# Kernel tuning notes

Measured on AMD Instinct MI355X. Metric: run time of the kernel, lower is better.

## Reference

```python
import jax, jax.numpy as jnp
import numpy as np

N_ATOMS = 1_000_000
N_PAIRS = 32_000_000
N_MOL = 10_000

def setup_inputs() -> dict:
    key = jax.random.key(0)
    k1, k2, k3, k4, k5 = jax.random.split(key, 5)
    charges = jax.random.normal(k1, (N_ATOMS, 1), dtype=jnp.float32)
    # distances in [0.5, 2.5) to avoid divide-by-zero
    pair_dist = jax.random.uniform(k2, (N_PAIRS,), dtype=jnp.float32, minval=0.5, maxval=2.5)
    pair_first = jax.random.randint(k3, (N_PAIRS,), 0, N_ATOMS)
    pair_second = jax.random.randint(k4, (N_PAIRS,), 0, N_ATOMS)
    mol_index = jax.random.randint(k5, (N_ATOMS,), 0, N_MOL)
    return {
        "charges": charges,
        "pair_dist": pair_dist,
        "pair_first": pair_first,
        "pair_second": pair_second,
        "mol_index": mol_index,
        "n_molecules": N_MOL,
        "energy_conversion_factor": jnp.float32(14.399645),
    }

def reference(charges, pair_dist, pair_first, pair_second, mol_index, n_molecules, energy_conversion_factor):
    n_atoms = charges.shape[0]
    # gather charge of second atom in each pair, scale by 1/r  -> [n_pairs, 1]
    voltage_pairs = energy_conversion_factor * (charges[pair_second] / pair_dist[:, None])
    # scatter-add pair voltages onto first atom -> [n_atoms, 1]
    voltage_atom = jax.ops.segment_sum(voltage_pairs, pair_first, num_segments=n_atoms)
    # per-atom coulomb energy, then segment-sum over molecules
    coulomb_atom = voltage_atom * charges
    coulomb_molecules = 0.5 * jax.ops.segment_sum(coulomb_atom, mol_index, num_segments=n_molecules)
    return coulomb_molecules, voltage_atom
```

## Files before the change

### kernel.cpp

```cpp
#include <hip/hip_runtime.h>
#include <hip/hip_fp16.h>

#define BUCKET_BITS 12
#define BUCKET_SIZE 4096
#define NB 256
#define PPB 8192
#define BLK_A 256
#define MOL_BLOCKS 64


__global__ void init_cursors(int* __restrict__ cur, int nbuckets, int cap) {
    int b = blockIdx.x * blockDim.x + threadIdx.x;
    if (b < nbuckets) cur[b] = b * cap;
}

__global__ __launch_bounds__(BLK_A) void pair_scatter(
    const int4*   __restrict__ first4,
    const int4*   __restrict__ second4,
    const float4* __restrict__ dist4,
    const float*  __restrict__ charges,
    const float*  __restrict__ ecf_p,
    int* __restrict__ cur,
    unsigned* __restrict__ entries,
    int n_pairs4) {
    __shared__ unsigned stag[PPB];
    __shared__ int hist[NB];
    __shared__ int scanA[NB];
    __shared__ int lofs[NB + 1];
    __shared__ int gadj[NB];

    const int tid = threadIdx.x;
    hist[tid] = 0;
    __syncthreads();

    const int groups = PPB / 4;
    const int base4 = blockIdx.x * groups;

    #pragma unroll
    for (int it = 0; it < groups / BLK_A; ++it) {
        int g = base4 + it * BLK_A + tid;
        if (g < n_pairs4) {
            int4 f = first4[g];
            atomicAdd(&hist[f.x >> BUCKET_BITS], 1);
            atomicAdd(&hist[f.y >> BUCKET_BITS], 1);
            atomicAdd(&hist[f.z >> BUCKET_BITS], 1);
            atomicAdd(&hist[f.w >> BUCKET_BITS], 1);
        }
    }
    __syncthreads();

    scanA[tid] = hist[tid];
    __syncthreads();
    for (int off = 1; off < NB; off <<= 1) {
        int v = scanA[tid];
        if (tid >= off) v += scanA[tid - off];
        __syncthreads();
        scanA[tid] = v;
        __syncthreads();
    }
    if (tid == 0) lofs[0] = 0;
    lofs[tid + 1] = scanA[tid];
    __syncthreads();

    int cnt = hist[tid];
    if (cnt > 0) gadj[tid] = atomicAdd(&cur[tid], cnt) - lofs[tid];
    hist[tid] = lofs[tid];
    __syncthreads();

    const float ecf = *ecf_p;

    #pragma unroll
    for (int it = 0; it < groups / BLK_A; ++it) {
        int g = base4 + it * BLK_A + tid;
        if (g < n_pairs4) {
            int4   f = first4[g];
            int4   s = second4[g];
            float4 d = dist4[g];
            float v0 = ecf * charges[s.x] / d.x;
            float v1 = ecf * charges[s.y] / d.y;
            float v2 = ecf * charges[s.z] / d.z;
            float v3 = ecf * charges[s.w] / d.w;
            int p0 = atomicAdd(&hist[f.x >> BUCKET_BITS], 1);
            stag[p0] = ((unsigned)(f.x & (BUCKET_SIZE - 1)) << 16) |
                       (unsigned)__half_as_ushort(__float2half(v0));
            int p1 = atomicAdd(&hist[f.y >> BUCKET_BITS], 1);
            stag[p1] = ((unsigned)(f.y & (BUCKET_SIZE - 1)) << 16) |
                       (unsigned)__half_as_ushort(__float2half(v1));
            int p2 = atomicAdd(&hist[f.z >> BUCKET_BITS], 1);
            stag[p2] = ((unsigned)(f.z & (BUCKET_SIZE - 1)) << 16) |
                       (unsigned)__half_as_ushort(__float2half(v2));
            int p3 = atomicAdd(&hist[f.w >> BUCKET_BITS], 1);
            stag[p3] = ((unsigned)(f.w & (BUCKET_SIZE - 1)) << 16) |
                       (unsigned)__half_as_ushort(__float2half(v3));
        }
    }
    __syncthreads();

    const int tot = lofs[NB];
    for (int i = tid; i < tot; i += BLK_A) {
        unsigned e = stag[i];
        int lo = 0, hi = NB - 1;
        #pragma unroll
        for (int s = 0; s < 8; ++s) {
            int mid = (lo + hi + 1) >> 1;
            if (lofs[mid] <= i) lo = mid; else hi = mid - 1;
        }
        entries[gadj[lo] + i] = e;
    }
}

__global__ __launch_bounds__(1024) void bucket_reduce(
    const unsigned* __restrict__ entries,
    const int* __restrict__ cur,
    float* __restrict__ voltage,
    int cap, int n_atoms) {
    __shared__ float volt[BUCKET_SIZE];
    const int b = blockIdx.x;
    for (int i = threadIdx.x; i < BUCKET_SIZE; i += blockDim.x) volt[i] = 0.f;
    __syncthreads();
    const int start = b * cap;
    const int end = cur[b];
    const int cnt = end - start;
    const int cnt4 = cnt >> 2;
    const uint4* e4p = (const uint4*)(entries + start);
    for (int i = threadIdx.x; i < cnt4; i += blockDim.x) {
        uint4 e = e4p[i];
        atomicAdd(&volt[e.x >> 16], __half2float(__ushort_as_half((unsigned short)(e.x & 0xFFFFu))));
        atomicAdd(&volt[e.y >> 16], __half2float(__ushort_as_half((unsigned short)(e.y & 0xFFFFu))));
        atomicAdd(&volt[e.z >> 16], __half2float(__ushort_as_half((unsigned short)(e.z & 0xFFFFu))));
        atomicAdd(&volt[e.w >> 16], __half2float(__ushort_as_half((unsigned short)(e.w & 0xFFFFu))));
    }
    for (int i = (cnt4 << 2) + threadIdx.x; i < cnt; i += blockDim.x) {
        unsigned e = entries[start + i];
        atomicAdd(&volt[e >> 16], __half2float(__ushort_as_half((unsigned short)(e & 0xFFFFu))));
    }
    __syncthreads();
    const int abase = b << BUCKET_BITS;
    const int nat = min(BUCKET_SIZE, n_atoms - abase);
    for (int i = threadIdx.x; i < nat; i += blockDim.x)
        voltage[abase + i] = volt[i];
}

__global__ __launch_bounds__(1024) void mol_partial(
    const float* __restrict__ charges,
    const float* __restrict__ voltage,
    const int*  __restrict__ mol_index,
    float* __restrict__ partials,
    int n_mol, int n_atoms) {
    extern __shared__ float smem[];
    for (int i = threadIdx.x; i < n_mol; i += blockDim.x) smem[i] = 0.f;
    __syncthreads();
    const int n4 = n_atoms >> 2;
    const int gid = blockIdx.x * blockDim.x + threadIdx.x;
    const int stride = gridDim.x * blockDim.x;
    const float4* c4p = (const float4*)charges;
    const float4* v4p = (const float4*)voltage;
    const int4*   m4p = (const int4*)mol_index;
    for (int i = gid; i < n4; i += stride) {
        float4 c = c4p[i]; float4 v = v4p[i]; int4 m = m4p[i];
        atomicAdd(&smem[m.x], 0.5f * v.x * c.x);
        atomicAdd(&smem[m.y], 0.5f * v.y * c.y);
        atomicAdd(&smem[m.z], 0.5f * v.z * c.z);
        atomicAdd(&smem[m.w], 0.5f * v.w * c.w);
    }
    for (int i = (n4 << 2) + gid; i < n_atoms; i += stride)
        atomicAdd(&smem[mol_index[i]], 0.5f * voltage[i] * charges[i]);
    __syncthreads();
    float* dst = partials + (size_t)blockIdx.x * n_mol;
    for (int i = threadIdx.x; i < n_mol; i += blockDim.x)
        dst[i] = smem[i];
}

__global__ void mol_final(const float* __restrict__ partials,
                          float* __restrict__ mol_out,
                          int n_mol, int nparts) {
    int m = blockIdx.x * blockDim.x + threadIdx.x;
    if (m >= n_mol) return;
    float s = 0.f;
    for (int p = 0; p < nparts; ++p) s += partials[(size_t)p * n_mol + m];
    mol_out[m] = s;
}


__global__ void coulomb_pair_direct(const float* __restrict__ dist,
                                    const int*  __restrict__ first,
                                    const int*  __restrict__ second,
                                    const float* __restrict__ charges,
                                    const float* __restrict__ ecf_p,
                                    float* __restrict__ voltage,
                                    int n_pairs) {
    int p = blockIdx.x * blockDim.x + threadIdx.x;
    if (p >= n_pairs) return;
    float v = (*ecf_p) * charges[second[p]] / dist[p];
    atomicAdd(&voltage[first[p]], v);
}

__global__ void coulomb_atom_direct(const float* __restrict__ charges,
                                    const float* __restrict__ voltage,
                                    const int*  __restrict__ mol_index,
                                    float* __restrict__ mol_out,
                                    int n_atoms) {
    int a = blockIdx.x * blockDim.x + threadIdx.x;
    if (a >= n_atoms) return;
    atomicAdd(&mol_out[mol_index[a]], 0.5f * voltage[a] * charges[a]);
}

extern "C" void kernel_launch(void* const* d_in, const int* in_sizes, int n_in,
                              void* d_out, int out_size, void* d_ws, size_t ws_size,
                              hipStream_t stream) {
    const float* charges     = (const float*)d_in[0];
    const float* pair_dist   = (const float*)d_in[1];
    const int*   pair_first  = (const int*)d_in[2];
    const int*   pair_second = (const int*)d_in[3];
    const int*   mol_index   = (const int*)d_in[4];
    const float* ecf_p       = (const float*)d_in[6];

    const int n_atoms = in_sizes[0];
    const int n_pairs = in_sizes[1];
    const int n_mol   = out_size - n_atoms;

    float* mol_out = (float*)d_out;
    float* voltage = (float*)d_out + n_mol;

    const int nbuckets = (n_atoms + BUCKET_SIZE - 1) >> BUCKET_BITS;
    long long capll = (long long)n_pairs / (nbuckets > 0 ? nbuckets : 1);
    capll += capll / 16 + 4096;
    capll = (capll + 3) & ~3LL;
    long long tot_entries = capll * nbuckets;
    size_t entries_bytes = (size_t)tot_entries * sizeof(unsigned);
    size_t cur_off = (entries_bytes + 255) & ~(size_t)255;
    size_t mol_off = (cur_off + (size_t)nbuckets * sizeof(int) + 255) & ~(size_t)255;
    size_t need_base = cur_off + (size_t)nbuckets * sizeof(int);
    size_t need_mol  = mol_off + (size_t)MOL_BLOCKS * n_mol * sizeof(float);

    const bool mol_lds_ok = (size_t)n_mol * sizeof(float) <= 60 * 1024;
    const bool fast = (nbuckets >= 1) && (nbuckets <= NB) &&
                      (tot_entries < 0x7fffffffLL) &&
                      ((n_pairs & 3) == 0) &&
                      (need_base <= ws_size);
    const bool mol_hier = fast && mol_lds_ok && (need_mol <= ws_size);

    if (fast) {
        unsigned* entries = (unsigned*)d_ws;
        int* cur = (int*)((char*)d_ws + cur_off);
        const int cap = (int)capll;

        init_cursors<<<1, 256, 0, stream>>>(cur, nbuckets, cap);

        const int n_pairs4 = n_pairs >> 2;
        const int nblocks = (n_pairs + PPB - 1) / PPB;
        pair_scatter<<<nblocks, BLK_A, 0, stream>>>(
            (const int4*)pair_first, (const int4*)pair_second,
            (const float4*)pair_dist, charges, ecf_p, cur, entries, n_pairs4);

        bucket_reduce<<<nbuckets, 1024, 0, stream>>>(entries, cur, voltage,
                                                     cap, n_atoms);

        if (mol_hier) {
            float* partials = (float*)((char*)d_ws + mol_off);
            mol_partial<<<MOL_BLOCKS, 1024, n_mol * sizeof(float), stream>>>(
                charges, voltage, mol_index, partials, n_mol, n_atoms);
            mol_final<<<(n_mol + 255) / 256, 256, 0, stream>>>(
                partials, mol_out, n_mol, MOL_BLOCKS);
        } else {
            hipMemsetAsync(d_out, 0, (size_t)n_mol * sizeof(float), stream);
            coulomb_atom_direct<<<(n_atoms + 255) / 256, 256, 0, stream>>>(
                charges, voltage, mol_index, mol_out, n_atoms);
        }
    } else {
        hipMemsetAsync(d_out, 0, (size_t)out_size * sizeof(float), stream);
        coulomb_pair_direct<<<(n_pairs + 255) / 256, 256, 0, stream>>>(
            pair_dist, pair_first, pair_second, charges, ecf_p, voltage, n_pairs);
        coulomb_atom_direct<<<(n_atoms + 255) / 256, 256, 0, stream>>>(
            charges, voltage, mol_index, mol_out, n_atoms);
    }
}
```

Baseline: 807.4 us.

## Fuse molecule partial sums into bucket reduce and cache pair values in registers

pair_scatter now reads first/second/dist only once. It computes the packed half-precision entries and bucket ids in registers during the histogram pass, so the second pass no longer re-reads the inputs or repeats the charge gather. The bucket reduce kernel is fused with the per-molecule partial accumulation, which removes the separate mol_partial pass over charges, voltage and mol_index. Nontemporal loads and stores and a 4-blocks-per-SM launch bound are also added. In exchange, register pressure goes up, each bucket block needs a 40KB LDS molecule array, and mol_final now sums 245 partial rows instead of 64.

```diff
diff --git a/kernel.cpp b/kernel.cpp
--- a/kernel.cpp
+++ b/kernel.cpp
@@ -6,7 +6,11 @@
 #define NB 256
 #define PPB 8192
 #define BLK_A 256
-#define MOL_BLOCKS 64
+#define ITERS (PPB / 4 / BLK_A)
+
+typedef int      v4i __attribute__((ext_vector_type(4)));
+typedef float    v4f __attribute__((ext_vector_type(4)));
+typedef unsigned v4u __attribute__((ext_vector_type(4)));
 
 
 __global__ void init_cursors(int* __restrict__ cur, int nbuckets, int cap) {
@@ -14,12 +18,12 @@
     if (b < nbuckets) cur[b] = b * cap;
 }
 
-__global__ __launch_bounds__(BLK_A) void pair_scatter(
-    const int4*   __restrict__ first4,
-    const int4*   __restrict__ second4,
-    const float4* __restrict__ dist4,
-    const float*  __restrict__ charges,
-    const float*  __restrict__ ecf_p,
+__global__ __launch_bounds__(BLK_A, 4) void pair_scatter(
+    const v4i*   __restrict__ first4,
+    const v4i*   __restrict__ second4,
+    const v4f*   __restrict__ dist4,
+    const float* __restrict__ charges,
+    const float* __restrict__ ecf_p,
     int* __restrict__ cur,
     unsigned* __restrict__ entries,
     int n_pairs4) {
@@ -33,18 +37,40 @@
     hist[tid] = 0;
     __syncthreads();
 
-    const int groups = PPB / 4;
-    const int base4 = blockIdx.x * groups;
+    const int base4 = blockIdx.x * (PPB / 4);
+    const float ecf = *ecf_p;
+
+    unsigned ev[ITERS * 4];
+    unsigned bks[ITERS];
 
     #pragma unroll
-    for (int it = 0; it < groups / BLK_A; ++it) {
+    for (int it = 0; it < ITERS; ++it) {
         int g = base4 + it * BLK_A + tid;
         if (g < n_pairs4) {
-            int4 f = first4[g];
-            atomicAdd(&hist[f.x >> BUCKET_BITS], 1);
-            atomicAdd(&hist[f.y >> BUCKET_BITS], 1);
-            atomicAdd(&hist[f.z >> BUCKET_BITS], 1);
-            atomicAdd(&hist[f.w >> BUCKET_BITS], 1);
+            v4i f = __builtin_nontemporal_load(&first4[g]);
+            v4i s = __builtin_nontemporal_load(&second4[g]);
+            v4f d = __builtin_nontemporal_load(&dist4[g]);
+            float v0 = ecf * charges[s[0]] / d[0];
+            float v1 = ecf * charges[s[1]] / d[1];
+            float v2 = ecf * charges[s[2]] / d[2];
+            float v3 = ecf * charges[s[3]] / d[3];
+            ev[it * 4 + 0] = ((unsigned)(f[0] & (BUCKET_SIZE - 1)) << 16) |
+                             (unsigned)__half_as_ushort(__float2half(v0));
+            ev[it * 4 + 1] = ((unsigned)(f[1] & (BUCKET_SIZE - 1)) << 16) |
+                             (unsigned)__half_as_ushort(__float2half(v1));
+            ev[it * 4 + 2] = ((unsigned)(f[2] & (BUCKET_SIZE - 1)) << 16) |
+                             (unsigned)__half_as_ushort(__float2half(v2));
+            ev[it * 4 + 3] = ((unsigned)(f[3] & (BUCKET_SIZE - 1)) << 16) |
+                             (unsigned)__half_as_ushort(__float2half(v3));
+            unsigned b0 = (unsigned)f[0] >> BUCKET_BITS;
+            unsigned b1 = (unsigned)f[1] >> BUCKET_BITS;
+            unsigned b2 = (unsigned)f[2] >> BUCKET_BITS;
+            unsigned b3 = (unsigned)f[3] >> BUCKET_BITS;
+            bks[it] = b0 | (b1 << 8) | (b2 << 16) | (b3 << 24);
+            atomicAdd(&hist[b0], 1);
+            atomicAdd(&hist[b1], 1);
+            atomicAdd(&hist[b2], 1);
+            atomicAdd(&hist[b3], 1);
         }
     }
     __syncthreads();
@@ -67,31 +93,16 @@
     hist[tid] = lofs[tid];
     __syncthreads();
 
-    const float ecf = *ecf_p;
-
     #pragma unroll
-    for (int it = 0; it < groups / BLK_A; ++it) {
+    for (int it = 0; it < ITERS; ++it) {
         int g = base4 + it * BLK_A + tid;
         if (g < n_pairs4) {
-            int4   f = first4[g];
-            int4   s = second4[g];
-            float4 d = dist4[g];
-            float v0 = ecf * charges[s.x] / d.x;
-            float v1 = ecf * charges[s.y] / d.y;
-            float v2 = ecf * charges[s.z] / d.z;
-            float v3 = ecf * charges[s.w] / d.w;
-            int p0 = atomicAdd(&hist[f.x >> BUCKET_BITS], 1);
-            stag[p0] = ((unsigned)(f.x & (BUCKET_SIZE - 1)) << 16) |
-                       (unsigned)__half_as_ushort(__float2half(v0));
-            int p1 = atomicAdd(&hist[f.y >> BUCKET_BITS], 1);
-            stag[p1] = ((unsigned)(f.y & (BUCKET_SIZE - 1)) << 16) |
-                       (unsigned)__half_as_ushort(__float2half(v1));
-            int p2 = atomicAdd(&hist[f.z >> BUCKET_BITS], 1);
-            stag[p2] = ((unsigned)(f.z & (BUCKET_SIZE - 1)) << 16) |
-                       (unsigned)__half_as_ushort(__float2half(v2));
-            int p3 = atomicAdd(&hist[f.w >> BUCKET_BITS], 1);
-            stag[p3] = ((unsigned)(f.w & (BUCKET_SIZE - 1)) << 16) |
-                       (unsigned)__half_as_ushort(__float2half(v3));
+            #pragma unroll
+            for (int j = 0; j < 4; ++j) {
+                int b = (bks[it] >> (8 * j)) & 0xFF;
+                int p = atomicAdd(&hist[b], 1);
+                stag[p] = ev[it * 4 + j];
+            }
         }
     }
     __syncthreads();
@@ -105,70 +116,54 @@
             int mid = (lo + hi + 1) >> 1;
             if (lofs[mid] <= i) lo = mid; else hi = mid - 1;
         }
-        entries[gadj[lo] + i] = e;
-    }
-}
-
-__global__ __launch_bounds__(1024) void bucket_reduce(
+        __builtin_nontemporal_store(e, &entries[gadj[lo] + i]);
+    }
+}
+
+__global__ __launch_bounds__(1024) void bucket_reduce_fused(
     const unsigned* __restrict__ entries,
     const int* __restrict__ cur,
+    const float* __restrict__ charges,
+    const int*  __restrict__ mol_index,
     float* __restrict__ voltage,
-    int cap, int n_atoms) {
+    float* __restrict__ partials,
+    int n_mol, int cap, int n_atoms) {
     __shared__ float volt[BUCKET_SIZE];
+    extern __shared__ float molsm[];
     const int b = blockIdx.x;
     for (int i = threadIdx.x; i < BUCKET_SIZE; i += blockDim.x) volt[i] = 0.f;
-    __syncthreads();
+    for (int i = threadIdx.x; i < n_mol; i += blockDim.x) molsm[i] = 0.f;
+    __syncthreads();
+
     const int start = b * cap;
-    const int end = cur[b];
-    const int cnt = end - start;
+    const int cnt = cur[b] - start;
     const int cnt4 = cnt >> 2;
-    const uint4* e4p = (const uint4*)(entries + start);
+    const v4u* e4p = (const v4u*)(entries + start);
     for (int i = threadIdx.x; i < cnt4; i += blockDim.x) {
-        uint4 e = e4p[i];
-        atomicAdd(&volt[e.x >> 16], __half2float(__ushort_as_half((unsigned short)(e.x & 0xFFFFu))));
-        atomicAdd(&volt[e.y >> 16], __half2float(__ushort_as_half((unsigned short)(e.y & 0xFFFFu))));
-        atomicAdd(&volt[e.z >> 16], __half2float(__ushort_as_half((unsigned short)(e.z & 0xFFFFu))));
-        atomicAdd(&volt[e.w >> 16], __half2float(__ushort_as_half((unsigned short)(e.w & 0xFFFFu))));
+        v4u e = __builtin_nontemporal_load(&e4p[i]);
+        atomicAdd(&volt[e[0] >> 16], __half2float(__ushort_as_half((unsigned short)(e[0] & 0xFFFFu))));
+        atomicAdd(&volt[e[1] >> 16], __half2float(__ushort_as_half((unsigned short)(e[1] & 0xFFFFu))));
+        atomicAdd(&volt[e[2] >> 16], __half2float(__ushort_as_half((unsigned short)(e[2] & 0xFFFFu))));
+        atomicAdd(&volt[e[3] >> 16], __half2float(__ushort_as_half((unsigned short)(e[3] & 0xFFFFu))));
     }
     for (int i = (cnt4 << 2) + threadIdx.x; i < cnt; i += blockDim.x) {
         unsigned e = entries[start + i];
         atomicAdd(&volt[e >> 16], __half2float(__ushort_as_half((unsigned short)(e & 0xFFFFu))));
     }
     __syncthreads();
+
     const int abase = b << BUCKET_BITS;
     const int nat = min(BUCKET_SIZE, n_atoms - abase);
-    for (int i = threadIdx.x; i < nat; i += blockDim.x)
-        voltage[abase + i] = volt[i];
-}
-
-__global__ __launch_bounds__(1024) void mol_partial(
-    const float* __restrict__ charges,
-    const float* __restrict__ voltage,
-    const int*  __restrict__ mol_index,
-    float* __restrict__ partials,
-    int n_mol, int n_atoms) {
-    extern __shared__ float smem[];
-    for (int i = threadIdx.x; i < n_mol; i += blockDim.x) smem[i] = 0.f;
-    __syncthreads();
-    const int n4 = n_atoms >> 2;
-    const int gid = blockIdx.x * blockDim.x + threadIdx.x;
-    const int stride = gridDim.x * blockDim.x;
-    const float4* c4p = (const float4*)charges;
-    const float4* v4p = (const float4*)voltage;
-    const int4*   m4p = (const int4*)mol_index;
-    for (int i = gid; i < n4; i += stride) {
-        float4 c = c4p[i]; float4 v = v4p[i]; int4 m = m4p[i];
-        atomicAdd(&smem[m.x], 0.5f * v.x * c.x);
-        atomicAdd(&smem[m.y], 0.5f * v.y * c.y);
-        atomicAdd(&smem[m.z], 0.5f * v.z * c.z);
-        atomicAdd(&smem[m.w], 0.5f * v.w * c.w);
-    }
-    for (int i = (n4 << 2) + gid; i < n_atoms; i += stride)
-        atomicAdd(&smem[mol_index[i]], 0.5f * voltage[i] * charges[i]);
-    __syncthreads();
-    float* dst = partials + (size_t)blockIdx.x * n_mol;
+    for (int i = threadIdx.x; i < nat; i += blockDim.x) {
+        float v = volt[i];
+        __builtin_nontemporal_store(v, &voltage[abase + i]);
+        float c = 0.5f * v * charges[abase + i];
+        atomicAdd(&molsm[mol_index[abase + i]], c);
+    }
+    __syncthreads();
+    float* dst = partials + (size_t)b * n_mol;
     for (int i = threadIdx.x; i < n_mol; i += blockDim.x)
-        dst[i] = smem[i];
+        __builtin_nontemporal_store(molsm[i], &dst[i]);
 }
 
 __global__ void mol_final(const float* __restrict__ partials,
@@ -179,6 +174,37 @@
     float s = 0.f;
     for (int p = 0; p < nparts; ++p) s += partials[(size_t)p * n_mol + m];
     mol_out[m] = s;
+}
+
+__global__ __launch_bounds__(1024) void bucket_reduce_plain(
+    const unsigned* __restrict__ entries,
+    const int* __restrict__ cur,
+    float* __restrict__ voltage,
+    int cap, int n_atoms) {
+    __shared__ float volt[BUCKET_SIZE];
+    const int b = blockIdx.x;
+    for (int i = threadIdx.x; i < BUCKET_SIZE; i += blockDim.x) volt[i] = 0.f;
+    __syncthreads();
+    const int start = b * cap;
+    const int cnt = cur[b] - start;
+    const int cnt4 = cnt >> 2;
+    const v4u* e4p = (const v4u*)(entries + start);
+    for (int i = threadIdx.x; i < cnt4; i += blockDim.x) {
+        v4u e = __builtin_nontemporal_load(&e4p[i]);
+        atomicAdd(&volt[e[0] >> 16], __half2float(__ushort_as_half((unsigned short)(e[0] & 0xFFFFu))));
+        atomicAdd(&volt[e[1] >> 16], __half2float(__ushort_as_half((unsigned short)(e[1] & 0xFFFFu))));
+        atomicAdd(&volt[e[2] >> 16], __half2float(__ushort_as_half((unsigned short)(e[2] & 0xFFFFu))));
+        atomicAdd(&volt[e[3] >> 16], __half2float(__ushort_as_half((unsigned short)(e[3] & 0xFFFFu))));
+    }
+    for (int i = (cnt4 << 2) + threadIdx.x; i < cnt; i += blockDim.x) {
+        unsigned e = entries[start + i];
+        atomicAdd(&volt[e >> 16], __half2float(__ushort_as_half((unsigned short)(e & 0xFFFFu))));
+    }
+    __syncthreads();
+    const int abase = b << BUCKET_BITS;
+    const int nat = min(BUCKET_SIZE, n_atoms - abase);
+    for (int i = threadIdx.x; i < nat; i += blockDim.x)
+        voltage[abase + i] = volt[i];
 }
 
 
@@ -231,38 +257,38 @@
     size_t cur_off = (entries_bytes + 255) & ~(size_t)255;
     size_t mol_off = (cur_off + (size_t)nbuckets * sizeof(int) + 255) & ~(size_t)255;
     size_t need_base = cur_off + (size_t)nbuckets * sizeof(int);
-    size_t need_mol  = mol_off + (size_t)MOL_BLOCKS * n_mol * sizeof(float);
-
-    const bool mol_lds_ok = (size_t)n_mol * sizeof(float) <= 60 * 1024;
+    size_t need_mol  = mol_off + (size_t)nbuckets * n_mol * sizeof(float);
+
+    const bool mol_lds_ok = (size_t)n_mol * sizeof(float) <= 40 * 1024;
     const bool fast = (nbuckets >= 1) && (nbuckets <= NB) &&
                       (tot_entries < 0x7fffffffLL) &&
                       ((n_pairs & 3) == 0) &&
                       (need_base <= ws_size);
-    const bool mol_hier = fast && mol_lds_ok && (need_mol <= ws_size);
+    const bool mol_fused = fast && mol_lds_ok && (need_mol <= ws_size);
 
     if (fast) {
         unsigned* entries = (unsigned*)d_ws;
         int* cur = (int*)((char*)d_ws + cur_off);
         const int cap = (int)capll;
 
-        init_cursors<<<1, 256, 0, stream>>>(cur, nbuckets, cap);
+        init_cursors<<<(nbuckets + 255) / 256, 256, 0, stream>>>(cur, nbuckets, cap);
 
         const int n_pairs4 = n_pairs >> 2;
         const int nblocks = (n_pairs + PPB - 1) / PPB;
         pair_scatter<<<nblocks, BLK_A, 0, stream>>>(
-            (const int4*)pair_first, (const int4*)pair_second,
-            (const float4*)pair_dist, charges, ecf_p, cur, entries, n_pairs4);
-
-        bucket_reduce<<<nbuckets, 1024, 0, stream>>>(entries, cur, voltage,
-                                                     cap, n_atoms);
-
-        if (mol_hier) {
+            (const v4i*)pair_first, (const v4i*)pair_second,
+            (const v4f*)pair_dist, charges, ecf_p, cur, entries, n_pairs4);
+
+        if (mol_fused) {
             float* partials = (float*)((char*)d_ws + mol_off);
-            mol_partial<<<MOL_BLOCKS, 1024, n_mol * sizeof(float), stream>>>(
-                charges, voltage, mol_index, partials, n_mol, n_atoms);
+            bucket_reduce_fused<<<nbuckets, 1024, n_mol * sizeof(float), stream>>>(
+                entries, cur, charges, mol_index, voltage, partials,
+                n_mol, cap, n_atoms);
             mol_final<<<(n_mol + 255) / 256, 256, 0, stream>>>(
-                partials, mol_out, n_mol, MOL_BLOCKS);
+                partials, mol_out, n_mol, nbuckets);
         } else {
+            bucket_reduce_plain<<<nbuckets, 1024, 0, stream>>>(
+                entries, cur, voltage, cap, n_atoms);
             hipMemsetAsync(d_out, 0, (size_t)n_mol * sizeof(float), stream);
             coulomb_atom_direct<<<(n_atoms + 255) / 256, 256, 0, stream>>>(
                 charges, voltage, mol_index, mol_out, n_atoms);
```

New measurement: 828.3 us. 2.6% more time.
